# Optimization experiments

Hardware: AMD Instinct MI355X
Metric: run time of the kernel (lower is better)

## Reference

```python
import jax, jax.numpy as jnp
import numpy as np

B = 512
DIM_X = 128
DIM_Y = 128
HIDDEN = 512


def setup_inputs() -> dict:
    key = jax.random.key(0)
    kx, ky, kw1, kw2 = jax.random.split(key, 4)
    x = jax.random.normal(kx, (B, DIM_X), dtype=jnp.float32)
    y = jax.random.normal(ky, (B, DIM_Y), dtype=jnp.float32)
    # Glorot-ish scaling for the Dense layers
    W1 = jax.random.normal(kw1, (DIM_X + DIM_Y, HIDDEN), dtype=jnp.float32) * (1.0 / np.sqrt(DIM_X + DIM_Y))
    b1 = jnp.zeros((HIDDEN,), dtype=jnp.float32)
    W2 = jax.random.normal(kw2, (HIDDEN, 1), dtype=jnp.float32) * (1.0 / np.sqrt(HIDDEN))
    b2 = jnp.zeros((1,), dtype=jnp.float32)
    return {"x": x, "y": y, "W1": W1, "b1": b1, "W2": W2, "b2": b2}


def reference(x, y, W1, b1, W2, b2):
    # scores[i, j] = f(concat(x_i, y_j)) with f = Dense(512, relu) -> Dense(1).
    # Since the first Dense is linear in the concatenated input, split W1 into
    # the x-block and y-block and broadcast-sum instead of materializing the
    # [B*B, dim_x+dim_y] concat tensor (same math as tile+concat+matmul).
    dim_x = x.shape[1]
    hx = x @ W1[:dim_x]          # [B, H]
    hy = y @ W1[dim_x:]          # [B, H]
    h = jax.nn.relu(hx[:, None, :] + hy[None, :, :] + b1)  # [B, B, H]
    scores = jnp.einsum('ijh,h->ij', h, W2[:, 0]) + b2[0]   # [B, B]
    return scores
```

## Files before the change

kernel.cpp:

```cpp
#include <hip/hip_runtime.h>


#define BATCH 512
#define DX    128
#define HID   512

typedef _Float16 half2_t __attribute__((ext_vector_type(2)));

static __device__ __forceinline__ half2_t u2h(unsigned int u) {
    union { unsigned int u; half2_t h; } c; c.u = u; return c.h;
}
static __device__ __forceinline__ unsigned int h2u(half2_t h) {
    union { half2_t h; unsigned int u; } c; c.h = h; return c.u;
}

__global__ __launch_bounds__(256) void proj_kernel(
    const float* __restrict__ x, const float* __restrict__ y,
    const float* __restrict__ W1, const float* __restrict__ b1,
    _Float16* __restrict__ hxy)
{
    const int part = blockIdx.y;
    const int row0 = blockIdx.x * 8;
    const int h    = blockIdx.z * 256 + threadIdx.x;
    const float* __restrict__ src = part ? y : x;
    const float* __restrict__ W   = W1 + part * DX * HID;

    __shared__ float s[8][DX];
    {
        const int t = threadIdx.x;
        const int r = t >> 5, c4 = (t & 31) << 2;
        const float4 v = *(const float4*)&src[(row0 + r) * DX + c4];
        s[r][c4] = v.x; s[r][c4 + 1] = v.y; s[r][c4 + 2] = v.z; s[r][c4 + 3] = v.w;
    }
    __syncthreads();

    float acc[8] = {0.f, 0.f, 0.f, 0.f, 0.f, 0.f, 0.f, 0.f};
    #pragma unroll 4
    for (int k = 0; k < DX; ++k) {
        const float w = W[k * HID + h];
        #pragma unroll
        for (int r = 0; r < 8; ++r) acc[r] = fmaf(s[r][k], w, acc[r]);
    }
    const float bias = part ? b1[h] : 0.0f;
    #pragma unroll
    for (int r = 0; r < 8; ++r)
        hxy[(part * BATCH + row0 + r) * HID + h] = (_Float16)(acc[r] + bias);
}

#define TI   64
#define TJ   32
#define HC   64
#define HPW  (HC / 2)
#define TS   33

__global__ __launch_bounds__(256, 4) void score_kernel(
    const _Float16* __restrict__ hxy, const float* __restrict__ W2,
    const float* __restrict__ b2, float* __restrict__ out)
{
    __shared__ unsigned int sAu[TI * TS];
    __shared__ unsigned int sBu[TJ * TS];
    __shared__ unsigned int sWu[HPW];

    const int i0 = blockIdx.y * TI;
    const int j0 = blockIdx.x * TJ;
    const int h0 = blockIdx.z * HC;
    const int tid = threadIdx.x;

    {
        #pragma unroll
        for (int it = 0; it < 2; ++it) {
            const int s = tid + 256 * it;
            const int row = s >> 3, q = s & 7;
            const uint4 v = *(const uint4*)&hxy[(i0 + row) * HID + h0 + (q << 3)];
            unsigned int* p = &sAu[row * TS + (q << 2)];
            p[0] = v.x; p[1] = v.y; p[2] = v.z; p[3] = v.w;
        }
        {
            const int row = tid >> 3, q = tid & 7;
            const uint4 v = *(const uint4*)&hxy[(BATCH + j0 + row) * HID + h0 + (q << 3)];
            unsigned int* p = &sBu[row * TS + (q << 2)];
            p[0] = v.x; p[1] = v.y; p[2] = v.z; p[3] = v.w;
        }
        if (tid < HPW) {
            const float2 w = *(const float2*)&W2[h0 + 2 * tid];
            half2_t wh;
            wh.x = (_Float16)w.x;
            wh.y = (_Float16)w.y;
            sWu[tid] = h2u(wh);
        }
    }
    __syncthreads();

    const int tx = tid & 15;
    const int ty = tid >> 4;
    const unsigned int* pa = &sAu[(4 * ty) * TS];
    const unsigned int* pb = &sBu[(2 * tx) * TS];

    float acc[4][2] = {{0.f,0.f},{0.f,0.f},{0.f,0.f},{0.f,0.f}};
    const half2_t hz = {(_Float16)0, (_Float16)0};

    #pragma unroll 8
    for (int hp = 0; hp < HPW; ++hp) {
        const half2_t w  = u2h(sWu[hp]);
        const half2_t a0 = u2h(pa[hp]);
        const half2_t a1 = u2h(pa[TS + hp]);
        const half2_t a2 = u2h(pa[2 * TS + hp]);
        const half2_t a3 = u2h(pa[3 * TS + hp]);
        const half2_t b0 = u2h(pb[hp]);
        const half2_t b1v = u2h(pb[TS + hp]);
        half2_t a[4] = {a0, a1, a2, a3};
        half2_t b[2] = {b0, b1v};
        #pragma unroll
        for (int r = 0; r < 4; ++r)
            #pragma unroll
            for (int c = 0; c < 2; ++c) {
                half2_t t = a[r] + b[c];
                t = __builtin_elementwise_max(t, hz);
                acc[r][c] = __builtin_amdgcn_fdot2(t, w, acc[r][c], false);
            }
    }

    const float bs = (blockIdx.z == 0) ? b2[0] : 0.0f;
    const int i = i0 + 4 * ty;
    const int j = j0 + 2 * tx;
    #pragma unroll
    for (int r = 0; r < 4; ++r) {
        atomicAdd(&out[(i + r) * BATCH + j],     acc[r][0] + bs);
        atomicAdd(&out[(i + r) * BATCH + j + 1], acc[r][1] + bs);
    }
}

extern "C" void kernel_launch(void* const* d_in, const int* in_sizes, int n_in,
                              void* d_out, int out_size, void* d_ws, size_t ws_size,
                              hipStream_t stream) {
    const float* x  = (const float*)d_in[0];
    const float* y  = (const float*)d_in[1];
    const float* W1 = (const float*)d_in[2];
    const float* b1 = (const float*)d_in[3];
    const float* W2 = (const float*)d_in[4];
    const float* b2 = (const float*)d_in[5];
    float* out = (float*)d_out;
    _Float16* hxy = (_Float16*)d_ws;

    (void)hipMemsetAsync(out, 0, BATCH * BATCH * sizeof(float), stream);
    proj_kernel<<<dim3(BATCH / 8, 2, 2), 256, 0, stream>>>(x, y, W1, b1, hxy);
    score_kernel<<<dim3(BATCH / TJ, BATCH / TI, HID / HC), 256, 0, stream>>>(hxy, W2, b2, out);
}
```

Before: 93.15 us.

## Enlarge score tiles and replace atomic accumulation with partial buffers plus reduce

The score kernel now uses 128x64 tiles with 512 threads, and each thread computes a 4x4 output block instead of 4x2, which raises register-level reuse of the A and B loads. Instead of atomically adding into a memset output, each hidden-chunk writes its partial scores to a separate workspace slice with float4 stores. A new reduce kernel sums the 8 slices and adds the bias. This removes the memset and the atomic contention, at the cost of an extra 8 MB of partial-buffer traffic and a third launch.

```diff
diff --git a/kernel.cpp b/kernel.cpp
--- a/kernel.cpp
+++ b/kernel.cpp
@@ -47,87 +47,99 @@
         hxy[(part * BATCH + row0 + r) * HID + h] = (_Float16)(acc[r] + bias);
 }
 
-#define TI   64
-#define TJ   32
+#define TI   128
+#define TJ   64
 #define HC   64
 #define HPW  (HC / 2)
-#define TS   33
+#define ST   33
 
-__global__ __launch_bounds__(256, 4) void score_kernel(
+__global__ __launch_bounds__(512, 2) void score_kernel(
     const _Float16* __restrict__ hxy, const float* __restrict__ W2,
-    const float* __restrict__ b2, float* __restrict__ out)
+    float* __restrict__ pws)
 {
-    __shared__ unsigned int sAu[TI * TS];
-    __shared__ unsigned int sBu[TJ * TS];
-    __shared__ unsigned int sWu[HPW];
+    __shared__ unsigned int sA[TI * ST];
+    __shared__ unsigned int sB[TJ * ST];
+    __shared__ unsigned int sW[HPW];
 
     const int i0 = blockIdx.y * TI;
     const int j0 = blockIdx.x * TJ;
-    const int h0 = blockIdx.z * HC;
+    const int hp0 = blockIdx.z * HPW;
     const int tid = threadIdx.x;
+    const unsigned int* __restrict__ hx32 = (const unsigned int*)hxy;
 
+    #pragma unroll
+    for (int it = 0; it < 2; ++it) {
+        const int s = tid + it * 512;
+        const int row = s >> 3, q = s & 7;
+        const uint4 v = *(const uint4*)&hx32[(i0 + row) * 256 + hp0 + (q << 2)];
+        unsigned int* p = &sA[row * ST + (q << 2)];
+        p[0] = v.x; p[1] = v.y; p[2] = v.z; p[3] = v.w;
+    }
     {
-        #pragma unroll
-        for (int it = 0; it < 2; ++it) {
-            const int s = tid + 256 * it;
-            const int row = s >> 3, q = s & 7;
-            const uint4 v = *(const uint4*)&hxy[(i0 + row) * HID + h0 + (q << 3)];
-            unsigned int* p = &sAu[row * TS + (q << 2)];
-            p[0] = v.x; p[1] = v.y; p[2] = v.z; p[3] = v.w;
-        }
-        {
-            const int row = tid >> 3, q = tid & 7;
-            const uint4 v = *(const uint4*)&hxy[(BATCH + j0 + row) * HID + h0 + (q << 3)];
-            unsigned int* p = &sBu[row * TS + (q << 2)];
-            p[0] = v.x; p[1] = v.y; p[2] = v.z; p[3] = v.w;
-        }
-        if (tid < HPW) {
-            const float2 w = *(const float2*)&W2[h0 + 2 * tid];
-            half2_t wh;
-            wh.x = (_Float16)w.x;
-            wh.y = (_Float16)w.y;
-            sWu[tid] = h2u(wh);
-        }
+        const int row = tid >> 3, q = tid & 7;
+        const uint4 v = *(const uint4*)&hx32[(BATCH + j0 + row) * 256 + hp0 + (q << 2)];
+        unsigned int* p = &sB[row * ST + (q << 2)];
+        p[0] = v.x; p[1] = v.y; p[2] = v.z; p[3] = v.w;
+    }
+    if (tid < HPW) {
+        const float2 w = *(const float2*)&W2[2 * (hp0 + tid)];
+        half2_t wh; wh.x = (_Float16)w.x; wh.y = (_Float16)w.y;
+        sW[tid] = h2u(wh);
     }
     __syncthreads();
 
     const int tx = tid & 15;
     const int ty = tid >> 4;
-    const unsigned int* pa = &sAu[(4 * ty) * TS];
-    const unsigned int* pb = &sBu[(2 * tx) * TS];
+    const unsigned int* pa = &sA[(ty << 2) * ST];
+    const unsigned int* pb = &sB[(tx << 2) * ST];
 
-    float acc[4][2] = {{0.f,0.f},{0.f,0.f},{0.f,0.f},{0.f,0.f}};
+    float acc[4][4] = {{0.f,0.f,0.f,0.f},{0.f,0.f,0.f,0.f},
+                       {0.f,0.f,0.f,0.f},{0.f,0.f,0.f,0.f}};
     const half2_t hz = {(_Float16)0, (_Float16)0};
 
-    #pragma unroll 8
+    #pragma unroll 4
     for (int hp = 0; hp < HPW; ++hp) {
-        const half2_t w  = u2h(sWu[hp]);
-        const half2_t a0 = u2h(pa[hp]);
-        const half2_t a1 = u2h(pa[TS + hp]);
-        const half2_t a2 = u2h(pa[2 * TS + hp]);
-        const half2_t a3 = u2h(pa[3 * TS + hp]);
-        const half2_t b0 = u2h(pb[hp]);
-        const half2_t b1v = u2h(pb[TS + hp]);
-        half2_t a[4] = {a0, a1, a2, a3};
-        half2_t b[2] = {b0, b1v};
+        const half2_t w = u2h(sW[hp]);
+        half2_t a[4], b[4];
+        #pragma unroll
+        for (int r = 0; r < 4; ++r) a[r] = u2h(pa[r * ST + hp]);
+        #pragma unroll
+        for (int c = 0; c < 4; ++c) b[c] = u2h(pb[c * ST + hp]);
         #pragma unroll
         for (int r = 0; r < 4; ++r)
             #pragma unroll
-            for (int c = 0; c < 2; ++c) {
+            for (int c = 0; c < 4; ++c) {
                 half2_t t = a[r] + b[c];
                 t = __builtin_elementwise_max(t, hz);
                 acc[r][c] = __builtin_amdgcn_fdot2(t, w, acc[r][c], false);
             }
     }
 
-    const float bs = (blockIdx.z == 0) ? b2[0] : 0.0f;
-    const int i = i0 + 4 * ty;
-    const int j = j0 + 2 * tx;
+    float* dst = pws + blockIdx.z * (BATCH * BATCH);
+    const int i = i0 + (ty << 2);
+    const int j = j0 + (tx << 2);
     #pragma unroll
     for (int r = 0; r < 4; ++r) {
-        atomicAdd(&out[(i + r) * BATCH + j],     acc[r][0] + bs);
-        atomicAdd(&out[(i + r) * BATCH + j + 1], acc[r][1] + bs);
+        float4 v = make_float4(acc[r][0], acc[r][1], acc[r][2], acc[r][3]);
+        *(float4*)&dst[(i + r) * BATCH + j] = v;
     }
+}
+
+__global__ __launch_bounds__(256) void reduce_kernel(
+    const float* __restrict__ pws, const float* __restrict__ b2,
+    float* __restrict__ out)
+{
+    const int idx4 = blockIdx.x * 256 + threadIdx.x;
+    const float4* __restrict__ p4 = (const float4*)pws;
+    float4 s = p4[idx4];
+    #pragma unroll
+    for (int z = 1; z < 8; ++z) {
+        const float4 v = p4[z * (BATCH * BATCH / 4) + idx4];
+        s.x += v.x; s.y += v.y; s.z += v.z; s.w += v.w;
+    }
+    const float bs = b2[0];
+    s.x += bs; s.y += bs; s.z += bs; s.w += bs;
+    ((float4*)out)[idx4] = s;
 }
 
 extern "C" void kernel_launch(void* const* d_in, const int* in_sizes, int n_in,
@@ -140,9 +152,11 @@
     const float* W2 = (const float*)d_in[4];
     const float* b2 = (const float*)d_in[5];
     float* out = (float*)d_out;
+
     _Float16* hxy = (_Float16*)d_ws;
+    float* pws = (float*)((char*)d_ws + (1 << 20));
 
-    (void)hipMemsetAsync(out, 0, BATCH * BATCH * sizeof(float), stream);
     proj_kernel<<<dim3(BATCH / 8, 2, 2), 256, 0, stream>>>(x, y, W1, b1, hxy);
-    score_kernel<<<dim3(BATCH / TJ, BATCH / TI, HID / HC), 256, 0, stream>>>(hxy, W2, b2, out);
+    score_kernel<<<dim3(BATCH / TJ, BATCH / TI, HID / HC), 512, 0, stream>>>(hxy, W2, pws);
+    reduce_kernel<<<dim3(BATCH * BATCH / 4 / 256), 256, 0, stream>>>(pws, b2, out);
 }
```

Result: faster. 88.71 us (-4.8%).
